# Kernel tuning notes

Hardware: AMD Instinct MI355X
Metric: run time of the kernel (lower is better)

The kernel has to match this reference:

```python
import jax, jax.numpy as jnp
import numpy as np

B, G, CIN, COUT = 1024, 64, 512, 512  # G = s**(num_layers-1) = 2**6


def setup_inputs() -> dict:
    key = jax.random.key(0)
    kx, kw = jax.random.split(key)
    x = jax.random.normal(kx, (B, G, CIN), dtype=jnp.float32)
    weight = jax.random.normal(kw, (G, CIN, COUT), dtype=jnp.float32)
    return {"x": x, "weight": weight}


def reference(x, weight):
    # Original: (x[:,:,:,None] * W[None]).sum(2) / sqrt(Cin), then sum over groups.
    # Fused equivalent: grouped contraction over (g, c) -> [B, Cout].
    scale = 1.0 / jnp.sqrt(jnp.asarray(x.shape[2], dtype=x.dtype))
    out = jnp.einsum("bgc,gco->bo", x, weight) * scale
    return out
```

## Files before the change

### kernel.cpp

```cpp
#include <hip/hip_runtime.h>
#include <hip/hip_bf16.h>

typedef __bf16 bf16x8 __attribute__((ext_vector_type(8)));
typedef float  f32x4  __attribute__((ext_vector_type(4)));

#define B_SZ    1024
#define COUT_SZ 512
#define K_SZ    32768
#define TM 128
#define TN 128
#define BK 32

__device__ __forceinline__ void async_copy16(const void* g, void* l) {
  __builtin_amdgcn_global_load_lds(
      (const __attribute__((address_space(1))) unsigned int*)g,
      (__attribute__((address_space(3))) unsigned int*)l, 16, 0, 0);
}

__global__ __launch_bounds__(256) void wtrans_kernel(
    const float* __restrict__ w, __bf16* __restrict__ wt) {
  __shared__ __bf16 t[64 * 72];
  const int kb = blockIdx.x * 64;
  const int ob = blockIdx.y * 64;
  const int tid = threadIdx.x;

  const int o4 = (tid & 15) * 4;
  const int k0 = (tid >> 4) * 4;
  const float* src = w + (size_t)(kb + k0) * COUT_SZ + ob + o4;
  f32x4 v0 = *(const f32x4*)(src);
  f32x4 v1 = *(const f32x4*)(src + COUT_SZ);
  f32x4 v2 = *(const f32x4*)(src + 2 * COUT_SZ);
  f32x4 v3 = *(const f32x4*)(src + 3 * COUT_SZ);
#pragma unroll
  for (int c = 0; c < 4; ++c) {
    union { __bf16 h[4]; unsigned long long u; } p;
    p.h[0] = (__bf16)v0[c]; p.h[1] = (__bf16)v1[c];
    p.h[2] = (__bf16)v2[c]; p.h[3] = (__bf16)v3[c];
    *(unsigned long long*)&t[(o4 + c) * 72 + k0] = p.u;
  }
  __syncthreads();

  const int o  = tid >> 2;
  const int kc = (tid & 3) * 16;
  const uint4* s0 = (const uint4*)&t[o * 72 + kc];
  uint4 a = s0[0];
  uint4 b = s0[1];
  uint4* dst = (uint4*)(wt + (size_t)(ob + o) * K_SZ + kb + kc);
  dst[0] = a;
  dst[1] = b;
}

__global__ __launch_bounds__(256, 4)
void gemm_kernel(const float* __restrict__ x, const __bf16* __restrict__ wt,
                 float* __restrict__ dst, int kchunk) {
  __shared__ float  As[TM * BK];
  __shared__ __bf16 Bs[TN * BK];

  const int lin = blockIdx.x;
  const int m0 = (lin & 7) * TM;
  const int n0 = ((lin >> 3) & 3) * TN;
  const int z  = lin >> 5;
  const int tid  = threadIdx.x;
  const int wave = tid >> 6;
  const int lane = tid & 63;

  const int kbase = z * kchunk;

  const int aRow = lane >> 3;
  const int aCh  = (lane & 7) ^ (aRow & 7);
  const float* ag0 = x + (size_t)(m0 + (wave * 4 + 0) * 8 + aRow) * K_SZ + kbase + aCh * 4;
  const float* ag1 = x + (size_t)(m0 + (wave * 4 + 1) * 8 + aRow) * K_SZ + kbase + aCh * 4;
  const float* ag2 = x + (size_t)(m0 + (wave * 4 + 2) * 8 + aRow) * K_SZ + kbase + aCh * 4;
  const float* ag3 = x + (size_t)(m0 + (wave * 4 + 3) * 8 + aRow) * K_SZ + kbase + aCh * 4;
  const int bRow = lane >> 2;
  const int bCh  = (lane & 3) ^ ((lane >> 3) & 3);
  const __bf16* bg0 = wt + (size_t)(n0 + (wave * 2 + 0) * 16 + bRow) * K_SZ + kbase + bCh * 8;
  const __bf16* bg1 = wt + (size_t)(n0 + (wave * 2 + 1) * 16 + bRow) * K_SZ + kbase + bCh * 8;

  float* aL0 = &As[(wave * 4 + 0) * 256];
  float* aL1 = &As[(wave * 4 + 1) * 256];
  float* aL2 = &As[(wave * 4 + 2) * 256];
  float* aL3 = &As[(wave * 4 + 3) * 256];
  __bf16* bL0 = &Bs[(wave * 2 + 0) * 512];
  __bf16* bL1 = &Bs[(wave * 2 + 1) * 512];

  const int lm = lane & 15;
  const int q  = lane >> 4;
  const int wm = (wave & 1) * 64;
  const int wn = (wave >> 1) * 64;

  const int aPcLo = (2 * q) ^ (lm & 7);
  const int bPc   = q ^ ((lm >> 1) & 3);

  f32x4 acc[4][4];
#pragma unroll
  for (int i = 0; i < 4; ++i)
#pragma unroll
    for (int j = 0; j < 4; ++j)
      acc[i][j] = (f32x4){0.f, 0.f, 0.f, 0.f};

  const int niter = kchunk / BK;
  for (int it = 0; it < niter; ++it) {
    async_copy16(ag0, aL0);
    async_copy16(ag1, aL1);
    async_copy16(ag2, aL2);
    async_copy16(ag3, aL3);
    async_copy16(bg0, bL0);
    async_copy16(bg1, bL1);
    ag0 += BK; ag1 += BK; ag2 += BK; ag3 += BK;
    bg0 += BK; bg1 += BK;
    __syncthreads();

    bf16x8 af[4], bfr[4];
#pragma unroll
    for (int i = 0; i < 4; ++i) {
      const float* rowp = &As[(wm + i * 16 + lm) * BK];
      f32x4 lo = *(const f32x4*)(rowp + aPcLo * 4);
      f32x4 hi = *(const f32x4*)(rowp + (aPcLo ^ 1) * 4);
      bf16x8 a;
#pragma unroll
      for (int e = 0; e < 4; ++e) {
        a[e]     = (__bf16)lo[e];
        a[e + 4] = (__bf16)hi[e];
      }
      af[i] = a;
    }
#pragma unroll
    for (int j = 0; j < 4; ++j)
      bfr[j] = *(const bf16x8*)&Bs[(wn + j * 16 + lm) * BK + bPc * 8];

#pragma unroll
    for (int i = 0; i < 4; ++i)
#pragma unroll
      for (int j = 0; j < 4; ++j)
        acc[i][j] = __builtin_amdgcn_mfma_f32_16x16x32_bf16(af[i], bfr[j], acc[i][j], 0, 0, 0);

    __syncthreads();
  }

  float* outp = dst + (size_t)z * (B_SZ * COUT_SZ)
              + (size_t)(m0 + wm + q * 4) * COUT_SZ + (n0 + wn + lm);
#pragma unroll
  for (int i = 0; i < 4; ++i) {
#pragma unroll
    for (int r = 0; r < 4; ++r) {
      float* o2 = outp + (size_t)(i * 16 + r) * COUT_SZ;
#pragma unroll
      for (int j = 0; j < 4; ++j)
        o2[j * 16] = acc[i][j][r];
    }
  }
}

__global__ __launch_bounds__(256) void reduce_kernel(
    const float* __restrict__ p, float* __restrict__ out, int S, float scale) {
  const int i = (blockIdx.x * 256 + threadIdx.x) * 4;
  f32x4 s = (f32x4){0.f, 0.f, 0.f, 0.f};
  for (int zz = 0; zz < S; ++zz) {
    f32x4 v = *(const f32x4*)(p + (size_t)zz * (B_SZ * COUT_SZ) + i);
    s = s + v;
  }
  s = s * scale;
  *(f32x4*)(out + i) = s;
}

extern "C" void kernel_launch(void* const* d_in, const int* in_sizes, int n_in,
                              void* d_out, int out_size, void* d_ws, size_t ws_size,
                              hipStream_t stream) {
  const float* x = (const float*)d_in[0];
  const float* w = (const float*)d_in[1];
  float* out = (float*)d_out;

  const size_t wtB    = (size_t)COUT_SZ * K_SZ * sizeof(__bf16);
  const size_t sliceB = (size_t)B_SZ * COUT_SZ * sizeof(float);

  __bf16* wt = (__bf16*)d_ws;
  int S = 32;
  while (S > 1 && wtB + (size_t)S * sliceB > ws_size) S >>= 1;
  float* partials = (float*)((char*)d_ws + wtB);
  if (wtB + sliceB > ws_size) { partials = out; S = 1; }

  const float scale = 0.04419417382415922f;

  hipLaunchKernelGGL(wtrans_kernel, dim3(K_SZ / 64, COUT_SZ / 64), dim3(256), 0,
                     stream, w, wt);
  hipLaunchKernelGGL(gemm_kernel, dim3(32 * S), dim3(256), 0, stream,
                     x, wt, partials, K_SZ / S);
  hipLaunchKernelGGL(reduce_kernel, dim3(B_SZ * COUT_SZ / 1024), dim3(256), 0,
                     stream, partials, out, S, scale);
}
```

Before: 312.5 us.

## Enlarge GEMM tiles to 256x256 with double-buffered LDS and z-major block order

The split-K GEMM now uses 256x256 output tiles computed by 512-thread blocks, so each x tile is reused across twice as many output columns. This halves the repeated fp32 reads of x from global memory. LDS is double-buffered, so the next K slice's async loads are issued while MFMAs run on the current one, and blocks are ordered K-split-major. The weight transpose kernel is rewritten to stage fp32 through a padded shared tile, and the reduce loop is unrolled by two. In exchange, LDS use and register pressure rise, the grid shrinks to one block per CU, and the small-workspace fallback is removed.

```diff
diff --git a/kernel.cpp b/kernel.cpp
--- a/kernel.cpp
+++ b/kernel.cpp
@@ -2,13 +2,14 @@
 #include <hip/hip_bf16.h>
 
 typedef __bf16 bf16x8 __attribute__((ext_vector_type(8)));
+typedef __bf16 bf16x4 __attribute__((ext_vector_type(4)));
 typedef float  f32x4  __attribute__((ext_vector_type(4)));
 
 #define B_SZ    1024
 #define COUT_SZ 512
 #define K_SZ    32768
-#define TM 128
-#define TN 128
+#define TM 256
+#define TN 256
 #define BK 32
 
 __device__ __forceinline__ void async_copy16(const void* g, void* l) {
@@ -19,102 +20,111 @@
 
 __global__ __launch_bounds__(256) void wtrans_kernel(
     const float* __restrict__ w, __bf16* __restrict__ wt) {
-  __shared__ __bf16 t[64 * 72];
+  __shared__ float t[64 * 65];
   const int kb = blockIdx.x * 64;
   const int ob = blockIdx.y * 64;
   const int tid = threadIdx.x;
 
-  const int o4 = (tid & 15) * 4;
-  const int k0 = (tid >> 4) * 4;
-  const float* src = w + (size_t)(kb + k0) * COUT_SZ + ob + o4;
-  f32x4 v0 = *(const f32x4*)(src);
-  f32x4 v1 = *(const f32x4*)(src + COUT_SZ);
-  f32x4 v2 = *(const f32x4*)(src + 2 * COUT_SZ);
-  f32x4 v3 = *(const f32x4*)(src + 3 * COUT_SZ);
+  {
+    const int o4 = (tid & 15) * 4;
+    const int kr = tid >> 4;
+    const float* src = w + (size_t)(kb + kr) * COUT_SZ + ob + o4;
 #pragma unroll
-  for (int c = 0; c < 4; ++c) {
-    union { __bf16 h[4]; unsigned long long u; } p;
-    p.h[0] = (__bf16)v0[c]; p.h[1] = (__bf16)v1[c];
-    p.h[2] = (__bf16)v2[c]; p.h[3] = (__bf16)v3[c];
-    *(unsigned long long*)&t[(o4 + c) * 72 + k0] = p.u;
+    for (int i = 0; i < 4; ++i) {
+      f32x4 v = *(const f32x4*)(src + (size_t)(16 * i) * COUT_SZ);
+      *(f32x4*)&t[(kr + 16 * i) * 65 + o4] = v;
+    }
   }
   __syncthreads();
-
-  const int o  = tid >> 2;
-  const int kc = (tid & 3) * 16;
-  const uint4* s0 = (const uint4*)&t[o * 72 + kc];
-  uint4 a = s0[0];
-  uint4 b = s0[1];
-  uint4* dst = (uint4*)(wt + (size_t)(ob + o) * K_SZ + kb + kc);
-  dst[0] = a;
-  dst[1] = b;
+  {
+    const int k4 = (tid & 15) * 4;
+    const int orow = tid >> 4;
+#pragma unroll
+    for (int j = 0; j < 4; ++j) {
+      const int o = orow + 16 * j;
+      bf16x4 p;
+#pragma unroll
+      for (int e = 0; e < 4; ++e) p[e] = (__bf16)t[(k4 + e) * 65 + o];
+      *(bf16x4*)(wt + (size_t)(ob + o) * K_SZ + kb + k4) = p;
+    }
+  }
 }
 
-__global__ __launch_bounds__(256, 4)
+__global__ __launch_bounds__(512, 2)
 void gemm_kernel(const float* __restrict__ x, const __bf16* __restrict__ wt,
-                 float* __restrict__ dst, int kchunk) {
-  __shared__ float  As[TM * BK];
-  __shared__ __bf16 Bs[TN * BK];
+                 float* __restrict__ dst, int kchunk, int S) {
+  __shared__ float  Asm[2][TM * BK];
+  __shared__ __bf16 Bsm[2][TN * BK];
 
   const int lin = blockIdx.x;
-  const int m0 = (lin & 7) * TM;
-  const int n0 = ((lin >> 3) & 3) * TN;
-  const int z  = lin >> 5;
+  const int z = lin % S;
+  const int t = lin / S;
+  const int m0 = (t & 3) * TM;
+  const int n0 = (t >> 2) * TN;
   const int tid  = threadIdx.x;
-  const int wave = tid >> 6;
+  const int w    = tid >> 6;
   const int lane = tid & 63;
 
   const int kbase = z * kchunk;
 
   const int aRow = lane >> 3;
-  const int aCh  = (lane & 7) ^ (aRow & 7);
-  const float* ag0 = x + (size_t)(m0 + (wave * 4 + 0) * 8 + aRow) * K_SZ + kbase + aCh * 4;
-  const float* ag1 = x + (size_t)(m0 + (wave * 4 + 1) * 8 + aRow) * K_SZ + kbase + aCh * 4;
-  const float* ag2 = x + (size_t)(m0 + (wave * 4 + 2) * 8 + aRow) * K_SZ + kbase + aCh * 4;
-  const float* ag3 = x + (size_t)(m0 + (wave * 4 + 3) * 8 + aRow) * K_SZ + kbase + aCh * 4;
+  const int aCh  = (lane & 7) ^ aRow;
+  const float* ag0 = x + (size_t)(m0 + (w * 4 + 0) * 8 + aRow) * K_SZ + kbase + aCh * 4;
+  const float* ag1 = x + (size_t)(m0 + (w * 4 + 1) * 8 + aRow) * K_SZ + kbase + aCh * 4;
+  const float* ag2 = x + (size_t)(m0 + (w * 4 + 2) * 8 + aRow) * K_SZ + kbase + aCh * 4;
+  const float* ag3 = x + (size_t)(m0 + (w * 4 + 3) * 8 + aRow) * K_SZ + kbase + aCh * 4;
   const int bRow = lane >> 2;
   const int bCh  = (lane & 3) ^ ((lane >> 3) & 3);
-  const __bf16* bg0 = wt + (size_t)(n0 + (wave * 2 + 0) * 16 + bRow) * K_SZ + kbase + bCh * 8;
-  const __bf16* bg1 = wt + (size_t)(n0 + (wave * 2 + 1) * 16 + bRow) * K_SZ + kbase + bCh * 8;
-
-  float* aL0 = &As[(wave * 4 + 0) * 256];
-  float* aL1 = &As[(wave * 4 + 1) * 256];
-  float* aL2 = &As[(wave * 4 + 2) * 256];
-  float* aL3 = &As[(wave * 4 + 3) * 256];
-  __bf16* bL0 = &Bs[(wave * 2 + 0) * 512];
-  __bf16* bL1 = &Bs[(wave * 2 + 1) * 512];
+  const __bf16* bg0 = wt + (size_t)(n0 + (w * 2 + 0) * 16 + bRow) * K_SZ + kbase + bCh * 8;
+  const __bf16* bg1 = wt + (size_t)(n0 + (w * 2 + 1) * 16 + bRow) * K_SZ + kbase + bCh * 8;
 
   const int lm = lane & 15;
   const int q  = lane >> 4;
-  const int wm = (wave & 1) * 64;
-  const int wn = (wave >> 1) * 64;
-
+  const int wm = (w & 1) * 128;
+  const int wn = (w >> 1) * 64;
   const int aPcLo = (2 * q) ^ (lm & 7);
   const int bPc   = q ^ ((lm >> 1) & 3);
 
-  f32x4 acc[4][4];
+  f32x4 acc[8][4];
 #pragma unroll
-  for (int i = 0; i < 4; ++i)
+  for (int i = 0; i < 8; ++i)
 #pragma unroll
     for (int j = 0; j < 4; ++j)
       acc[i][j] = (f32x4){0.f, 0.f, 0.f, 0.f};
 
+  async_copy16(ag0, &Asm[0][(w * 4 + 0) * 256]);
+  async_copy16(ag1, &Asm[0][(w * 4 + 1) * 256]);
+  async_copy16(ag2, &Asm[0][(w * 4 + 2) * 256]);
+  async_copy16(ag3, &Asm[0][(w * 4 + 3) * 256]);
+  async_copy16(bg0, &Bsm[0][(w * 2 + 0) * 512]);
+  async_copy16(bg1, &Bsm[0][(w * 2 + 1) * 512]);
+  ag0 += BK; ag1 += BK; ag2 += BK; ag3 += BK; bg0 += BK; bg1 += BK;
+
   const int niter = kchunk / BK;
   for (int it = 0; it < niter; ++it) {
-    async_copy16(ag0, aL0);
-    async_copy16(ag1, aL1);
-    async_copy16(ag2, aL2);
-    async_copy16(ag3, aL3);
-    async_copy16(bg0, bL0);
-    async_copy16(bg1, bL1);
-    ag0 += BK; ag1 += BK; ag2 += BK; ag3 += BK;
-    bg0 += BK; bg1 += BK;
     __syncthreads();
+    const int p = it & 1;
+    if (it + 1 < niter) {
+      const int np = p ^ 1;
+      async_copy16(ag0, &Asm[np][(w * 4 + 0) * 256]);
+      async_copy16(ag1, &Asm[np][(w * 4 + 1) * 256]);
+      async_copy16(ag2, &Asm[np][(w * 4 + 2) * 256]);
+      async_copy16(ag3, &Asm[np][(w * 4 + 3) * 256]);
+      async_copy16(bg0, &Bsm[np][(w * 2 + 0) * 512]);
+      async_copy16(bg1, &Bsm[np][(w * 2 + 1) * 512]);
+      ag0 += BK; ag1 += BK; ag2 += BK; ag3 += BK; bg0 += BK; bg1 += BK;
+    }
 
-    bf16x8 af[4], bfr[4];
+    const float*  A_ = Asm[p];
+    const __bf16* B_ = Bsm[p];
+    bf16x8 bfr[4];
 #pragma unroll
-    for (int i = 0; i < 4; ++i) {
-      const float* rowp = &As[(wm + i * 16 + lm) * BK];
+    for (int j = 0; j < 4; ++j)
+      bfr[j] = *(const bf16x8*)&B_[(wn + j * 16 + lm) * BK + bPc * 8];
+
+#pragma unroll
+    for (int i = 0; i < 8; ++i) {
+      const float* rowp = &A_[(wm + i * 16 + lm) * BK];
       f32x4 lo = *(const f32x4*)(rowp + aPcLo * 4);
       f32x4 hi = *(const f32x4*)(rowp + (aPcLo ^ 1) * 4);
       bf16x8 a;
@@ -123,25 +133,16 @@
         a[e]     = (__bf16)lo[e];
         a[e + 4] = (__bf16)hi[e];
       }
-      af[i] = a;
-    }
-#pragma unroll
-    for (int j = 0; j < 4; ++j)
-      bfr[j] = *(const bf16x8*)&Bs[(wn + j * 16 + lm) * BK + bPc * 8];
-
-#pragma unroll
-    for (int i = 0; i < 4; ++i)
 #pragma unroll
       for (int j = 0; j < 4; ++j)
-        acc[i][j] = __builtin_amdgcn_mfma_f32_16x16x32_bf16(af[i], bfr[j], acc[i][j], 0, 0, 0);
-
-    __syncthreads();
+        acc[i][j] = __builtin_amdgcn_mfma_f32_16x16x32_bf16(a, bfr[j], acc[i][j], 0, 0, 0);
+    }
   }
 
   float* outp = dst + (size_t)z * (B_SZ * COUT_SZ)
               + (size_t)(m0 + wm + q * 4) * COUT_SZ + (n0 + wn + lm);
 #pragma unroll
-  for (int i = 0; i < 4; ++i) {
+  for (int i = 0; i < 8; ++i) {
 #pragma unroll
     for (int r = 0; r < 4; ++r) {
       float* o2 = outp + (size_t)(i * 16 + r) * COUT_SZ;
@@ -155,13 +156,17 @@
 __global__ __launch_bounds__(256) void reduce_kernel(
     const float* __restrict__ p, float* __restrict__ out, int S, float scale) {
   const int i = (blockIdx.x * 256 + threadIdx.x) * 4;
-  f32x4 s = (f32x4){0.f, 0.f, 0.f, 0.f};
-  for (int zz = 0; zz < S; ++zz) {
-    f32x4 v = *(const f32x4*)(p + (size_t)zz * (B_SZ * COUT_SZ) + i);
-    s = s + v;
+  f32x4 s0 = (f32x4){0.f, 0.f, 0.f, 0.f};
+  f32x4 s1 = (f32x4){0.f, 0.f, 0.f, 0.f};
+  int zz = 0;
+  for (; zz + 1 < S; zz += 2) {
+    s0 = s0 + *(const f32x4*)(p + (size_t)zz * (B_SZ * COUT_SZ) + i);
+    s1 = s1 + *(const f32x4*)(p + (size_t)(zz + 1) * (B_SZ * COUT_SZ) + i);
   }
-  s = s * scale;
-  *(f32x4*)(out + i) = s;
+  for (; zz < S; ++zz)
+    s0 = s0 + *(const f32x4*)(p + (size_t)zz * (B_SZ * COUT_SZ) + i);
+  s0 = (s0 + s1) * scale;
+  *(f32x4*)(out + i) = s0;
 }
 
 extern "C" void kernel_launch(void* const* d_in, const int* in_sizes, int n_in,
@@ -178,14 +183,13 @@
   int S = 32;
   while (S > 1 && wtB + (size_t)S * sliceB > ws_size) S >>= 1;
   float* partials = (float*)((char*)d_ws + wtB);
-  if (wtB + sliceB > ws_size) { partials = out; S = 1; }
 
   const float scale = 0.04419417382415922f;
 
   hipLaunchKernelGGL(wtrans_kernel, dim3(K_SZ / 64, COUT_SZ / 64), dim3(256), 0,
                      stream, w, wt);
-  hipLaunchKernelGGL(gemm_kernel, dim3(32 * S), dim3(256), 0, stream,
-                     x, wt, partials, K_SZ / S);
+  hipLaunchKernelGGL(gemm_kernel, dim3(8 * S), dim3(512), 0, stream,
+                     x, wt, partials, K_SZ / S, S);
   hipLaunchKernelGGL(reduce_kernel, dim3(B_SZ * COUT_SZ / 1024), dim3(256), 0,
                      stream, partials, out, S, scale);
 }
```

New measurement: 302.2 us. -3.3%, faster.
